# Kernel tuning notes

Measured on AMD Instinct MI355X. Metric: run time of the kernel, lower is better.

## Reference

```python
import jax, jax.numpy as jnp
import numpy as np

NUM_EXPERTS = 8
TOP_K = 2
ROUTE_SCALE = 1.0
DIM = 1024
HID = 1024
B, S = 2, 4096


def setup_inputs() -> dict:
    key = jax.random.key(0)
    ks = jax.random.split(key, 9)
    sc = 0.05
    return {
        "x": jax.random.normal(ks[0], (B, S, DIM), dtype=jnp.float32),
        "gate_w": jax.random.normal(ks[1], (NUM_EXPERTS, DIM), dtype=jnp.float32) * sc,
        "w1": jax.random.normal(ks[2], (NUM_EXPERTS, HID, DIM), dtype=jnp.float32) * sc,
        "w2": jax.random.normal(ks[3], (NUM_EXPERTS, DIM, HID), dtype=jnp.float32) * sc,
        "w3": jax.random.normal(ks[4], (NUM_EXPERTS, HID, DIM), dtype=jnp.float32) * sc,
        "sw1": jax.random.normal(ks[5], (HID, DIM), dtype=jnp.float32) * sc,
        "sw2": jax.random.normal(ks[6], (DIM, HID), dtype=jnp.float32) * sc,
        "sw3": jax.random.normal(ks[7], (HID, DIM), dtype=jnp.float32) * sc,
        "expert_bias": jnp.zeros((NUM_EXPERTS,), dtype=jnp.float32),
    }


def reference(x, gate_w, w1, w2, w3, sw1, sw2, sw3, expert_bias):
    bs, slen, dim = x.shape
    xf = x.reshape(-1, dim)                      # [T, D]

    # ---- router (sigmoid scoring, top-k over scores + bias, gather true scores) ----
    scores = jax.nn.sigmoid((xf @ gate_w.T).astype(jnp.float32))   # [T, E]
    _, sel = jax.lax.top_k(scores + expert_bias[None, :], TOP_K)    # [T, K] int32
    top_scores = jnp.take_along_axis(scores, sel, axis=1) * ROUTE_SCALE  # [T, K]

    # ---- stable sort token-slots by chosen expert (dispatch permutation) ----
    flat_sel = sel.reshape(-1)                       # [T*K]
    order = jnp.argsort(flat_sel, stable=True)       # [T*K]
    scores_sorted = top_scores.reshape(-1)[order]    # [T*K]
    tok_idx = order // TOP_K                         # source token per slot
    expert_ids = flat_sel[order]                     # sorted expert id per slot

    routed = xf[tok_idx]                             # gather [T*K, D]
    # score_before_experts=True: scale inputs by routing score
    routed = (routed.astype(jnp.float32) * scores_sorted[:, None]).astype(x.dtype)

    # ---- grouped expert GLU MLP (loop over fixed expert count, masked) ----
    out_r = jnp.zeros_like(routed)
    for e in range(NUM_EXPERTS):
        m = (expert_ids == e)[:, None]
        h = jax.nn.silu(routed @ w1[e].T) * (routed @ w3[e].T)   # [T*K, H]
        out_r = out_r + jnp.where(m, h @ w2[e].T, jnp.zeros((), routed.dtype))

    # ---- shared expert on all tokens ----
    shared = (jax.nn.silu(xf @ sw1.T) * (xf @ sw3.T)) @ sw2.T    # [T, D]

    # NOTE: original code multiplies by routing scores again after experts
    # (in addition to score_before_experts) -- replicated faithfully.
    out_r = (out_r.astype(jnp.float32) * scores_sorted[:, None]).astype(x.dtype)

    out = shared.at[tok_idx].add(out_r)              # scatter-add combine
    return out.reshape(bs, slen, dim)
```

## Files before the change

### kernel.cpp

```cpp
#include <hip/hip_runtime.h>
#include <stdint.h>

typedef unsigned short u16;
typedef unsigned int u32;

#define T_TOK 8192
#define DIMSZ 1024
#define HIDSZ 1024
#define NE 8
#define NSLOT (T_TOK * 2)

typedef __attribute__((ext_vector_type(8))) __bf16 bf16x8;
typedef __attribute__((ext_vector_type(4))) float f32x4;

__device__ __forceinline__ int sw_idx(int row, int kc) {
  return row * 32 + ((kc ^ (row & 3)) * 8);
}

__device__ __forceinline__ u16 f2bf(float f) {
  u32 u = __builtin_bit_cast(u32, f);
  u += 0x7FFFu + ((u >> 16) & 1u);
  return (u16)(u >> 16);
}
__device__ __forceinline__ float bflo(u32 v) { return __builtin_bit_cast(float, v << 16); }
__device__ __forceinline__ float bfhi(u32 v) { return __builtin_bit_cast(float, v & 0xffff0000u); }
__device__ __forceinline__ u32 pack2(float a, float b) {
  return (u32)f2bf(a) | ((u32)f2bf(b) << 16);
}
__device__ __forceinline__ float silu_f(float v) { return v / (1.f + expf(-v)); }

__global__ __launch_bounds__(256) void convert3_kernel(
    const float* __restrict__ s0, const float* __restrict__ s1,
    const float* __restrict__ s2, u16* __restrict__ d0, u16* __restrict__ d1,
    u16* __restrict__ d2, int n4) {
  const float* s = (blockIdx.y == 0) ? s0 : (blockIdx.y == 1) ? s1 : s2;
  u16* d = (blockIdx.y == 0) ? d0 : (blockIdx.y == 1) ? d1 : d2;
  int stride = gridDim.x * 256;
  for (int i = blockIdx.x * 256 + threadIdx.x; i < n4; i += stride) {
    float4 v = ((const float4*)s)[i];
    uint2 p;
    p.x = pack2(v.x, v.y);
    p.y = pack2(v.z, v.w);
    ((uint2*)d)[i] = p;
  }
}

__global__ __launch_bounds__(256) void router_kernel(
    const float* __restrict__ x, const float* __restrict__ gw,
    const float* __restrict__ bias, int* __restrict__ sel,
    float* __restrict__ selscore, u16* __restrict__ xb) {
  int t = blockIdx.x * 4 + (threadIdx.x >> 6);
  int lane = threadIdx.x & 63;
  float a[NE];
#pragma unroll
  for (int e = 0; e < NE; e++) a[e] = 0.f;
#pragma unroll
  for (int j = 0; j < 4; j++) {
    int c = j * 256 + lane * 4;
    float4 xv = *(const float4*)&x[(size_t)t * DIMSZ + c];
    uint2 p;
    p.x = pack2(xv.x, xv.y);
    p.y = pack2(xv.z, xv.w);
    *(uint2*)&xb[(size_t)t * DIMSZ + c] = p;
#pragma unroll
    for (int e = 0; e < NE; e++) {
      float4 gv = *(const float4*)&gw[e * DIMSZ + c];
      a[e] = fmaf(xv.x, gv.x, fmaf(xv.y, gv.y, fmaf(xv.z, gv.z, fmaf(xv.w, gv.w, a[e]))));
    }
  }
#pragma unroll
  for (int off = 1; off < 64; off <<= 1)
#pragma unroll
    for (int e = 0; e < NE; e++) a[e] += __shfl_xor(a[e], off);
  if (lane == 0) {
    float s[NE], b[NE];
#pragma unroll
    for (int e = 0; e < NE; e++) {
      s[e] = 1.f / (1.f + expf(-a[e]));
      b[e] = s[e] + bias[e];
    }
    int e1 = 0; float v1 = b[0];
#pragma unroll
    for (int e = 1; e < NE; e++) if (b[e] > v1) { v1 = b[e]; e1 = e; }
    int e2 = -1; float v2 = -1e30f;
#pragma unroll
    for (int e = 0; e < NE; e++) if (e != e1 && b[e] > v2) { v2 = b[e]; e2 = e; }
    sel[t * 2] = e1; sel[t * 2 + 1] = e2;
    selscore[t * 2] = s[e1];
    selscore[t * 2 + 1] = s[e2];
  }
}

__global__ __launch_bounds__(1024) void rank_kernel(
    const int* __restrict__ sel, const float* __restrict__ selscore,
    int* __restrict__ slot2pos, float* __restrict__ slot_score,
    int* __restrict__ counts, int* __restrict__ offsets) {
  __shared__ int hist[NE * 1024];
  __shared__ int tot[NE];
  __shared__ int offs[NE];
  int tid = threadIdx.x;
  int sl[16];
  int h[NE];
#pragma unroll
  for (int e = 0; e < NE; e++) h[e] = 0;
#pragma unroll
  for (int j = 0; j < 4; j++) {
    int4 v = ((const int4*)sel)[tid * 4 + j];
    sl[j * 4 + 0] = v.x; sl[j * 4 + 1] = v.y;
    sl[j * 4 + 2] = v.z; sl[j * 4 + 3] = v.w;
  }
#pragma unroll
  for (int i = 0; i < 16; i++)
#pragma unroll
    for (int e = 0; e < NE; e++) h[e] += (sl[i] == e) ? 1 : 0;
#pragma unroll
  for (int e = 0; e < NE; e++) hist[e * 1024 + tid] = h[e];
  __syncthreads();
  int wid = tid >> 6, lane = tid & 63;
  if (wid < NE) {
    int e = wid;
    int vals[16];
    int lsum = 0;
#pragma unroll
    for (int i = 0; i < 16; i++) {
      int v = hist[e * 1024 + lane * 16 + i];
      vals[i] = lsum;
      lsum += v;
    }
    int incl = lsum;
#pragma unroll
    for (int off = 1; off < 64; off <<= 1) {
      int v = __shfl_up(incl, off);
      if (lane >= off) incl += v;
    }
    int excl = incl - lsum;
#pragma unroll
    for (int i = 0; i < 16; i++) hist[e * 1024 + lane * 16 + i] = vals[i] + excl;
    if (lane == 63) tot[e] = incl;
  }
  __syncthreads();
  if (tid == 0) {
    int acc = 0;
    for (int e = 0; e < NE; e++) {
      offs[e] = acc;
      offsets[e] = acc;
      counts[e] = tot[e];
      acc += tot[e];
    }
  }
  __syncthreads();
  int base[NE];
#pragma unroll
  for (int e = 0; e < NE; e++) base[e] = offs[e] + hist[e * 1024 + tid];
#pragma unroll
  for (int i = 0; i < 16; i++) {
    int slot = tid * 16 + i;
    int e = sl[i];
    int pos = 0;
#pragma unroll
    for (int k = 0; k < NE; k++) pos += (e == k) ? base[k] : 0;
#pragma unroll
    for (int k = 0; k < NE; k++) base[k] += (e == k) ? 1 : 0;
    slot2pos[slot] = pos;
    slot_score[pos] = selscore[slot];
  }
}

__global__ __launch_bounds__(256) void gather_kernel(
    const float* __restrict__ x, const float* __restrict__ selscore,
    const int* __restrict__ slot2pos, u16* __restrict__ routed) {
  int s = blockIdx.x * 4 + (threadIdx.x >> 6);
  int lane = threadIdx.x & 63;
  int pos = slot2pos[s];
  float sc = selscore[s];
  int t = s >> 1;
#pragma unroll
  for (int j = 0; j < 4; j++) {
    int c = j * 256 + lane * 4;
    float4 v = *(const float4*)&x[(size_t)t * DIMSZ + c];
    uint2 p;
    p.x = pack2(v.x * sc, v.y * sc);
    p.y = pack2(v.z * sc, v.w * sc);
    *(uint2*)&routed[(size_t)pos * DIMSZ + c] = p;
  }
}

__global__ __launch_bounds__(256) void dual_glu_gemm(
    const u16* __restrict__ A, const u16* __restrict__ W1,
    const u16* __restrict__ W3, u16* __restrict__ Hout,
    const int* __restrict__ seg_off, const int* __restrict__ seg_cnt, int fullM) {
  int z = blockIdx.z;
  int soff = 0, scnt = fullM;
  if (seg_off) { soff = seg_off[z]; scnt = seg_cnt[z]; }
  int mbase = blockIdx.y * 128;
  if (mbase >= scnt) return;
  int nbase = blockIdx.x * 64;
  const u16* w1p = W1 + (size_t)z * HIDSZ * DIMSZ;
  const u16* w3p = W3 + (size_t)z * HIDSZ * DIMSZ;

  __shared__ u16 lA[128 * 32];
  __shared__ u16 lB1[64 * 32];
  __shared__ u16 lB3[64 * 32];

  int tid = threadIdx.x;
  int lane = tid & 63;
  int wid = tid >> 6;
  int wy = wid >> 1, wx = wid & 1;
  int q = lane >> 4, lm = lane & 15;

  f32x4 acc1[4][2], acc3[4][2];
#pragma unroll
  for (int i = 0; i < 4; i++)
#pragma unroll
    for (int j = 0; j < 2; j++) { acc1[i][j] = (f32x4)0.f; acc3[i][j] = (f32x4)0.f; }

  int arow = tid >> 2, akc = tid & 3;
  int rg0 = min(mbase + arow, scnt - 1);
  int rg1 = min(mbase + arow + 64, scnt - 1);
  const u16* gA0 = A + (size_t)(soff + rg0) * DIMSZ + akc * 8;
  const u16* gA1 = A + (size_t)(soff + rg1) * DIMSZ + akc * 8;
  const u16* gB1 = w1p + (size_t)(nbase + arow) * DIMSZ + akc * 8;
  const u16* gB3 = w3p + (size_t)(nbase + arow) * DIMSZ + akc * 8;
  int sA0 = sw_idx(arow, akc), sA1 = sw_idx(arow + 64, akc);
  int sB = sw_idx(arow, akc);

  for (int kt = 0; kt < DIMSZ / 32; kt++) {
    uint4 vA0 = *(const uint4*)gA0;
    uint4 vA1 = *(const uint4*)gA1;
    uint4 vB1 = *(const uint4*)gB1;
    uint4 vB3 = *(const uint4*)gB3;
    gA0 += 32; gA1 += 32; gB1 += 32; gB3 += 32;
    *(uint4*)&lA[sA0] = vA0;
    *(uint4*)&lA[sA1] = vA1;
    *(uint4*)&lB1[sB] = vB1;
    *(uint4*)&lB3[sB] = vB3;
    __syncthreads();
    bf16x8 af[4];
#pragma unroll
    for (int i = 0; i < 4; i++) {
      int row = wy * 64 + i * 16 + lm;
      af[i] = *(const bf16x8*)&lA[sw_idx(row, q)];
    }
    bf16x8 b1f[2], b3f[2];
#pragma unroll
    for (int j = 0; j < 2; j++) {
      int col = wx * 32 + j * 16 + lm;
      b1f[j] = *(const bf16x8*)&lB1[sw_idx(col, q)];
      b3f[j] = *(const bf16x8*)&lB3[sw_idx(col, q)];
    }
#pragma unroll
    for (int i = 0; i < 4; i++)
#pragma unroll
      for (int j = 0; j < 2; j++) {
        acc1[i][j] = __builtin_amdgcn_mfma_f32_16x16x32_bf16(af[i], b1f[j], acc1[i][j], 0, 0, 0);
        acc3[i][j] = __builtin_amdgcn_mfma_f32_16x16x32_bf16(af[i], b3f[j], acc3[i][j], 0, 0, 0);
      }
    __syncthreads();
  }
#pragma unroll
  for (int i = 0; i < 4; i++) {
    int rowb = mbase + wy * 64 + i * 16 + q * 4;
#pragma unroll
    for (int j = 0; j < 2; j++) {
      int col = nbase + wx * 32 + j * 16 + lm;
      f32x4 g1 = acc1[i][j], g3 = acc3[i][j];
#pragma unroll
      for (int r = 0; r < 4; r++) {
        int grow = rowb + r;
        if (grow < scnt)
          Hout[(size_t)(soff + grow) * HIDSZ + col] = f2bf(silu_f(g1[r]) * g3[r]);
      }
    }
  }
}

template <bool OUT_BF16>
__global__ __launch_bounds__(256) void gemm2_kernel(
    const u16* __restrict__ A, const u16* __restrict__ W, void* __restrict__ Out,
    const float* __restrict__ scale, const int* __restrict__ seg_off,
    const int* __restrict__ seg_cnt, int fullM) {
  int z = blockIdx.z;
  int soff = 0, scnt = fullM;
  if (seg_off) { soff = seg_off[z]; scnt = seg_cnt[z]; }
  int mbase = blockIdx.y * 128;
  if (mbase >= scnt) return;
  int nbase = blockIdx.x * 128;
  const u16* wp = W + (size_t)z * DIMSZ * HIDSZ;

  __shared__ u16 lA[128 * 32];
  __shared__ u16 lB[128 * 32];

  int tid = threadIdx.x;
  int lane = tid & 63;
  int wid = tid >> 6;
  int wy = wid >> 1, wx = wid & 1;
  int q = lane >> 4, lm = lane & 15;

  f32x4 acc[4][4];
#pragma unroll
  for (int i = 0; i < 4; i++)
#pragma unroll
    for (int j = 0; j < 4; j++) acc[i][j] = (f32x4)0.f;

  int arow = tid >> 2, akc = tid & 3;
  int rg0 = min(mbase + arow, scnt - 1);
  int rg1 = min(mbase + arow + 64, scnt - 1);
  const u16* gA0 = A + (size_t)(soff + rg0) * HIDSZ + akc * 8;
  const u16* gA1 = A + (size_t)(soff + rg1) * HIDSZ + akc * 8;
  const u16* gB0 = wp + (size_t)(nbase + arow) * HIDSZ + akc * 8;
  const u16* gB1 = wp + (size_t)(nbase + arow + 64) * HIDSZ + akc * 8;
  int s0 = sw_idx(arow, akc), s1 = sw_idx(arow + 64, akc);

  for (int kt = 0; kt < HIDSZ / 32; kt++) {
    uint4 vA0 = *(const uint4*)gA0;
    uint4 vA1 = *(const uint4*)gA1;
    uint4 vB0 = *(const uint4*)gB0;
    uint4 vB1 = *(const uint4*)gB1;
    gA0 += 32; gA1 += 32; gB0 += 32; gB1 += 32;
    *(uint4*)&lA[s0] = vA0;
    *(uint4*)&lA[s1] = vA1;
    *(uint4*)&lB[s0] = vB0;
    *(uint4*)&lB[s1] = vB1;
    __syncthreads();
    bf16x8 af[4], bf[4];
#pragma unroll
    for (int i = 0; i < 4; i++) {
      int row = wy * 64 + i * 16 + lm;
      int col = wx * 64 + i * 16 + lm;
      af[i] = *(const bf16x8*)&lA[sw_idx(row, q)];
      bf[i] = *(const bf16x8*)&lB[sw_idx(col, q)];
    }
#pragma unroll
    for (int i = 0; i < 4; i++)
#pragma unroll
      for (int j = 0; j < 4; j++)
        acc[i][j] = __builtin_amdgcn_mfma_f32_16x16x32_bf16(af[i], bf[j], acc[i][j], 0, 0, 0);
    __syncthreads();
  }
#pragma unroll
  for (int i = 0; i < 4; i++) {
    int rowb = mbase + wy * 64 + i * 16 + q * 4;
#pragma unroll
    for (int j = 0; j < 4; j++) {
      int col = nbase + wx * 64 + j * 16 + lm;
      f32x4 a = acc[i][j];
#pragma unroll
      for (int r = 0; r < 4; r++) {
        int grow = rowb + r;
        if (grow < scnt) {
          float s = scale ? scale[soff + grow] : 1.f;
          float v = a[r] * s;
          size_t idx = (size_t)(soff + grow) * DIMSZ + col;
          if (OUT_BF16) ((u16*)Out)[idx] = f2bf(v);
          else ((float*)Out)[idx] = v;
        }
      }
    }
  }
}

__global__ __launch_bounds__(256) void combine_kernel(
    float* __restrict__ out, const u16* __restrict__ Orb,
    const int* __restrict__ slot2pos) {
  int t = blockIdx.x;
  int d = threadIdx.x * 4;
  int p0 = slot2pos[t * 2];
  int p1 = slot2pos[t * 2 + 1];
  float4 o = *(float4*)&out[(size_t)t * DIMSZ + d];
  uint2 a = *(const uint2*)&Orb[(size_t)p0 * DIMSZ + d];
  uint2 b = *(const uint2*)&Orb[(size_t)p1 * DIMSZ + d];
  o.x += bflo(a.x) + bflo(b.x);
  o.y += bfhi(a.x) + bfhi(b.x);
  o.z += bflo(a.y) + bflo(b.y);
  o.w += bfhi(a.y) + bfhi(b.y);
  *(float4*)&out[(size_t)t * DIMSZ + d] = o;
}

extern "C" void kernel_launch(void* const* d_in, const int* in_sizes, int n_in,
                              void* d_out, int out_size, void* d_ws, size_t ws_size,
                              hipStream_t stream) {
  const float* x = (const float*)d_in[0];
  const float* gw = (const float*)d_in[1];
  const float* w1 = (const float*)d_in[2];
  const float* w2 = (const float*)d_in[3];
  const float* w3 = (const float*)d_in[4];
  const float* sw1 = (const float*)d_in[5];
  const float* sw2 = (const float*)d_in[6];
  const float* sw3 = (const float*)d_in[7];
  const float* bias = (const float*)d_in[8];
  float* out = (float*)d_out;

  uint8_t* ws = (uint8_t*)d_ws;
  size_t off = 0;
  auto alloc = [&](size_t b) { size_t o = off; off += (b + 255) & ~(size_t)255; return o; };

  size_t ctrl = alloc(256);
  int* counts = (int*)(ws + ctrl);
  int* offsets = counts + 16;
  int* sel = (int*)(ws + alloc((size_t)NSLOT * 4));
  float* selscore = (float*)(ws + alloc((size_t)NSLOT * 4));
  float* slot_score = (float*)(ws + alloc((size_t)NSLOT * 4));
  int* slot2pos = (int*)(ws + alloc((size_t)NSLOT * 4));
  u16* xb = (u16*)(ws + alloc((size_t)T_TOK * DIMSZ * 2));
  u16* routed = (u16*)(ws + alloc((size_t)NSLOT * DIMSZ * 2));
  u16* Hbuf = (u16*)(ws + alloc((size_t)NSLOT * HIDSZ * 2));
  u16* Orb = (u16*)(ws + alloc((size_t)NSLOT * DIMSZ * 2));
  u16* Hs = (u16*)(ws + alloc((size_t)T_TOK * HIDSZ * 2));
  u16* w1b = (u16*)(ws + alloc((size_t)NE * HIDSZ * DIMSZ * 2));
  u16* w2b = (u16*)(ws + alloc((size_t)NE * DIMSZ * HIDSZ * 2));
  u16* w3b = (u16*)(ws + alloc((size_t)NE * HIDSZ * DIMSZ * 2));
  u16* sw1b = (u16*)(ws + alloc((size_t)HIDSZ * DIMSZ * 2));
  u16* sw2b = (u16*)(ws + alloc((size_t)DIMSZ * HIDSZ * 2));
  u16* sw3b = (u16*)(ws + alloc((size_t)HIDSZ * DIMSZ * 2));

  convert3_kernel<<<dim3(2048, 3), 256, 0, stream>>>(
      w1, w2, w3, w1b, w2b, w3b, NE * HIDSZ * DIMSZ / 4);
  convert3_kernel<<<dim3(512, 3), 256, 0, stream>>>(
      sw1, sw2, sw3, sw1b, sw2b, sw3b, HIDSZ * DIMSZ / 4);

  router_kernel<<<T_TOK / 4, 256, 0, stream>>>(x, gw, bias, sel, selscore, xb);
  rank_kernel<<<1, 1024, 0, stream>>>(sel, selscore, slot2pos, slot_score,
                                      counts, offsets);
  gather_kernel<<<NSLOT / 4, 256, 0, stream>>>(x, selscore, slot2pos, routed);

  dual_glu_gemm<<<dim3(16, 64, 8), 256, 0, stream>>>(routed, w1b, w3b, Hbuf,
                                                     offsets, counts, 0);
  gemm2_kernel<true><<<dim3(8, 64, 8), 256, 0, stream>>>(Hbuf, w2b, (void*)Orb,
                                                         slot_score, offsets, counts, 0);
  dual_glu_gemm<<<dim3(16, 64, 1), 256, 0, stream>>>(xb, sw1b, sw3b, Hs,
                                                     nullptr, nullptr, T_TOK);
  gemm2_kernel<false><<<dim3(8, 64, 1), 256, 0, stream>>>(Hs, sw2b, (void*)d_out,
                                                          nullptr, nullptr, nullptr, T_TOK);
  combine_kernel<<<T_TOK, 256, 0, stream>>>(out, Orb, slot2pos);
}
```

Before: 523.4 us.

## Merge shared expert into grouped GEMM launches, widen GLU tile, pad LDS layout

Result: slower. 627.8 us (+20.0%).

```diff
diff --git a/kernel.cpp b/kernel.cpp
--- a/kernel.cpp
+++ b/kernel.cpp
@@ -10,12 +10,10 @@
 #define NE 8
 #define NSLOT (T_TOK * 2)
 
+#define CS 1032
+
 typedef __attribute__((ext_vector_type(8))) __bf16 bf16x8;
 typedef __attribute__((ext_vector_type(4))) float f32x4;
-
-__device__ __forceinline__ int sw_idx(int row, int kc) {
-  return row * 32 + ((kc ^ (row & 3)) * 8);
-}
 
 __device__ __forceinline__ u16 f2bf(float f) {
   u32 u = __builtin_bit_cast(u32, f);
@@ -188,19 +186,29 @@
 __global__ __launch_bounds__(256) void dual_glu_gemm(
     const u16* __restrict__ A, const u16* __restrict__ W1,
     const u16* __restrict__ W3, u16* __restrict__ Hout,
-    const int* __restrict__ seg_off, const int* __restrict__ seg_cnt, int fullM) {
+    const u16* __restrict__ As, const u16* __restrict__ SW1,
+    const u16* __restrict__ SW3, u16* __restrict__ Hs,
+    const int* __restrict__ seg_off, const int* __restrict__ seg_cnt) {
   int z = blockIdx.z;
-  int soff = 0, scnt = fullM;
-  if (seg_off) { soff = seg_off[z]; scnt = seg_cnt[z]; }
+  const u16 *Ap, *w1p, *w3p;
+  u16* Hp;
+  int soff, scnt;
+  if (z < NE) {
+    soff = seg_off[z]; scnt = seg_cnt[z];
+    Ap = A; w1p = W1 + (size_t)z * HIDSZ * DIMSZ; w3p = W3 + (size_t)z * HIDSZ * DIMSZ;
+    Hp = Hout;
+  } else {
+    soff = 0; scnt = T_TOK;
+    Ap = As; w1p = SW1; w3p = SW3;
+    Hp = Hs;
+  }
   int mbase = blockIdx.y * 128;
   if (mbase >= scnt) return;
-  int nbase = blockIdx.x * 64;
-  const u16* w1p = W1 + (size_t)z * HIDSZ * DIMSZ;
-  const u16* w3p = W3 + (size_t)z * HIDSZ * DIMSZ;
-
-  __shared__ u16 lA[128 * 32];
-  __shared__ u16 lB1[64 * 32];
-  __shared__ u16 lB3[64 * 32];
+  int nbase = blockIdx.x * 128;
+
+  __shared__ u16 lA[4 * CS];
+  __shared__ u16 lB1[4 * CS];
+  __shared__ u16 lB3[4 * CS];
 
   int tid = threadIdx.x;
   int lane = tid & 63;
@@ -208,87 +216,93 @@
   int wy = wid >> 1, wx = wid & 1;
   int q = lane >> 4, lm = lane & 15;
 
-  f32x4 acc1[4][2], acc3[4][2];
+  f32x4 acc1[4][4], acc3[4][4];
 #pragma unroll
   for (int i = 0; i < 4; i++)
 #pragma unroll
-    for (int j = 0; j < 2; j++) { acc1[i][j] = (f32x4)0.f; acc3[i][j] = (f32x4)0.f; }
-
-  int arow = tid >> 2, akc = tid & 3;
-  int rg0 = min(mbase + arow, scnt - 1);
-  int rg1 = min(mbase + arow + 64, scnt - 1);
-  const u16* gA0 = A + (size_t)(soff + rg0) * DIMSZ + akc * 8;
-  const u16* gA1 = A + (size_t)(soff + rg1) * DIMSZ + akc * 8;
-  const u16* gB1 = w1p + (size_t)(nbase + arow) * DIMSZ + akc * 8;
-  const u16* gB3 = w3p + (size_t)(nbase + arow) * DIMSZ + akc * 8;
-  int sA0 = sw_idx(arow, akc), sA1 = sw_idx(arow + 64, akc);
-  int sB = sw_idx(arow, akc);
+    for (int j = 0; j < 4; j++) { acc1[i][j] = (f32x4)0.f; acc3[i][j] = (f32x4)0.f; }
+
+  int r = tid >> 2, kc = tid & 3;
+  int rg0 = min(mbase + r, scnt - 1);
+  int rg1 = min(mbase + r + 64, scnt - 1);
+  const u16* gA0 = Ap + (size_t)(soff + rg0) * DIMSZ + kc * 8;
+  const u16* gA1 = Ap + (size_t)(soff + rg1) * DIMSZ + kc * 8;
+  const u16* gB1a = w1p + (size_t)(nbase + r) * DIMSZ + kc * 8;
+  const u16* gB1b = w1p + (size_t)(nbase + r + 64) * DIMSZ + kc * 8;
+  const u16* gB3a = w3p + (size_t)(nbase + r) * DIMSZ + kc * 8;
+  const u16* gB3b = w3p + (size_t)(nbase + r + 64) * DIMSZ + kc * 8;
+  int s0 = kc * CS + r * 8, s1 = kc * CS + (r + 64) * 8;
 
   for (int kt = 0; kt < DIMSZ / 32; kt++) {
     uint4 vA0 = *(const uint4*)gA0;
     uint4 vA1 = *(const uint4*)gA1;
-    uint4 vB1 = *(const uint4*)gB1;
-    uint4 vB3 = *(const uint4*)gB3;
-    gA0 += 32; gA1 += 32; gB1 += 32; gB3 += 32;
-    *(uint4*)&lA[sA0] = vA0;
-    *(uint4*)&lA[sA1] = vA1;
-    *(uint4*)&lB1[sB] = vB1;
-    *(uint4*)&lB3[sB] = vB3;
+    uint4 vB1a = *(const uint4*)gB1a;
+    uint4 vB1b = *(const uint4*)gB1b;
+    uint4 vB3a = *(const uint4*)gB3a;
+    uint4 vB3b = *(const uint4*)gB3b;
+    gA0 += 32; gA1 += 32; gB1a += 32; gB1b += 32; gB3a += 32; gB3b += 32;
+    *(uint4*)&lA[s0] = vA0;
+    *(uint4*)&lA[s1] = vA1;
+    *(uint4*)&lB1[s0] = vB1a;
+    *(uint4*)&lB1[s1] = vB1b;
+    *(uint4*)&lB3[s0] = vB3a;
+    *(uint4*)&lB3[s1] = vB3b;
     __syncthreads();
     bf16x8 af[4];
 #pragma unroll
-    for (int i = 0; i < 4; i++) {
-      int row = wy * 64 + i * 16 + lm;
-      af[i] = *(const bf16x8*)&lA[sw_idx(row, q)];
-    }
-    bf16x8 b1f[2], b3f[2];
-#pragma unroll
-    for (int j = 0; j < 2; j++) {
-      int col = wx * 32 + j * 16 + lm;
-      b1f[j] = *(const bf16x8*)&lB1[sw_idx(col, q)];
-      b3f[j] = *(const bf16x8*)&lB3[sw_idx(col, q)];
-    }
-#pragma unroll
     for (int i = 0; i < 4; i++)
-#pragma unroll
-      for (int j = 0; j < 2; j++) {
-        acc1[i][j] = __builtin_amdgcn_mfma_f32_16x16x32_bf16(af[i], b1f[j], acc1[i][j], 0, 0, 0);
-        acc3[i][j] = __builtin_amdgcn_mfma_f32_16x16x32_bf16(af[i], b3f[j], acc3[i][j], 0, 0, 0);
+      af[i] = *(const bf16x8*)&lA[q * CS + (wy * 64 + i * 16 + lm) * 8];
+#pragma unroll
+    for (int j = 0; j < 4; j++) {
+      int col = wx * 64 + j * 16 + lm;
+      bf16x8 b1 = *(const bf16x8*)&lB1[q * CS + col * 8];
+      bf16x8 b3 = *(const bf16x8*)&lB3[q * CS + col * 8];
+#pragma unroll
+      for (int i = 0; i < 4; i++) {
+        acc1[i][j] = __builtin_amdgcn_mfma_f32_16x16x32_bf16(af[i], b1, acc1[i][j], 0, 0, 0);
+        acc3[i][j] = __builtin_amdgcn_mfma_f32_16x16x32_bf16(af[i], b3, acc3[i][j], 0, 0, 0);
       }
+    }
     __syncthreads();
   }
 #pragma unroll
   for (int i = 0; i < 4; i++) {
     int rowb = mbase + wy * 64 + i * 16 + q * 4;
 #pragma unroll
-    for (int j = 0; j < 2; j++) {
-      int col = nbase + wx * 32 + j * 16 + lm;
+    for (int j = 0; j < 4; j++) {
+      int col = nbase + wx * 64 + j * 16 + lm;
       f32x4 g1 = acc1[i][j], g3 = acc3[i][j];
 #pragma unroll
-      for (int r = 0; r < 4; r++) {
-        int grow = rowb + r;
+      for (int rr = 0; rr < 4; rr++) {
+        int grow = rowb + rr;
         if (grow < scnt)
-          Hout[(size_t)(soff + grow) * HIDSZ + col] = f2bf(silu_f(g1[r]) * g3[r]);
+          Hp[(size_t)(soff + grow) * HIDSZ + col] = f2bf(silu_f(g1[rr]) * g3[rr]);
       }
     }
   }
 }
 
-template <bool OUT_BF16>
 __global__ __launch_bounds__(256) void gemm2_kernel(
-    const u16* __restrict__ A, const u16* __restrict__ W, void* __restrict__ Out,
+    const u16* __restrict__ A, const u16* __restrict__ W, u16* __restrict__ OutB,
+    const u16* __restrict__ As, const u16* __restrict__ SW, float* __restrict__ OutF,
     const float* __restrict__ scale, const int* __restrict__ seg_off,
-    const int* __restrict__ seg_cnt, int fullM) {
+    const int* __restrict__ seg_cnt) {
   int z = blockIdx.z;
-  int soff = 0, scnt = fullM;
-  if (seg_off) { soff = seg_off[z]; scnt = seg_cnt[z]; }
+  const u16 *Ap, *wp;
+  int soff, scnt;
+  if (z < NE) {
+    soff = seg_off[z]; scnt = seg_cnt[z];
+    Ap = A; wp = W + (size_t)z * DIMSZ * HIDSZ;
+  } else {
+    soff = 0; scnt = T_TOK;
+    Ap = As; wp = SW;
+  }
   int mbase = blockIdx.y * 128;
   if (mbase >= scnt) return;
   int nbase = blockIdx.x * 128;
-  const u16* wp = W + (size_t)z * DIMSZ * HIDSZ;
-
-  __shared__ u16 lA[128 * 32];
-  __shared__ u16 lB[128 * 32];
+
+  __shared__ u16 lA[4 * CS];
+  __shared__ u16 lB[4 * CS];
 
   int tid = threadIdx.x;
   int lane = tid & 63;
@@ -302,14 +316,14 @@
 #pragma unroll
     for (int j = 0; j < 4; j++) acc[i][j] = (f32x4)0.f;
 
-  int arow = tid >> 2, akc = tid & 3;
-  int rg0 = min(mbase + arow, scnt - 1);
-  int rg1 = min(mbase + arow + 64, scnt - 1);
-  const u16* gA0 = A + (size_t)(soff + rg0) * HIDSZ + akc * 8;
-  const u16* gA1 = A + (size_t)(soff + rg1) * HIDSZ + akc * 8;
-  const u16* gB0 = wp + (size_t)(nbase + arow) * HIDSZ + akc * 8;
-  const u16* gB1 = wp + (size_t)(nbase + arow + 64) * HIDSZ + akc * 8;
-  int s0 = sw_idx(arow, akc), s1 = sw_idx(arow + 64, akc);
+  int r = tid >> 2, kc = tid & 3;
+  int rg0 = min(mbase + r, scnt - 1);
+  int rg1 = min(mbase + r + 64, scnt - 1);
+  const u16* gA0 = Ap + (size_t)(soff + rg0) * HIDSZ + kc * 8;
+  const u16* gA1 = Ap + (size_t)(soff + rg1) * HIDSZ + kc * 8;
+  const u16* gB0 = wp + (size_t)(nbase + r) * HIDSZ + kc * 8;
+  const u16* gB1 = wp + (size_t)(nbase + r + 64) * HIDSZ + kc * 8;
+  int s0 = kc * CS + r * 8, s1 = kc * CS + (r + 64) * 8;
 
   for (int kt = 0; kt < HIDSZ / 32; kt++) {
     uint4 vA0 = *(const uint4*)gA0;
@@ -325,10 +339,8 @@
     bf16x8 af[4], bf[4];
 #pragma unroll
     for (int i = 0; i < 4; i++) {
-      int row = wy * 64 + i * 16 + lm;
-      int col = wx * 64 + i * 16 + lm;
-      af[i] = *(const bf16x8*)&lA[sw_idx(row, q)];
-      bf[i] = *(const bf16x8*)&lB[sw_idx(col, q)];
+      af[i] = *(const bf16x8*)&lA[q * CS + (wy * 64 + i * 16 + lm) * 8];
+      bf[i] = *(const bf16x8*)&lB[q * CS + (wx * 64 + i * 16 + lm) * 8];
     }
 #pragma unroll
     for (int i = 0; i < 4; i++)
@@ -345,14 +357,15 @@
       int col = nbase + wx * 64 + j * 16 + lm;
       f32x4 a = acc[i][j];
 #pragma unroll
-      for (int r = 0; r < 4; r++) {
-        int grow = rowb + r;
+      for (int rr = 0; rr < 4; rr++) {
+        int grow = rowb + rr;
         if (grow < scnt) {
-          float s = scale ? scale[soff + grow] : 1.f;
-          float v = a[r] * s;
           size_t idx = (size_t)(soff + grow) * DIMSZ + col;
-          if (OUT_BF16) ((u16*)Out)[idx] = f2bf(v);
-          else ((float*)Out)[idx] = v;
+          if (z < NE) {
+            OutB[idx] = f2bf(a[rr] * scale[soff + grow]);
+          } else {
+            OutF[idx] = a[rr];
+          }
         }
       }
     }
@@ -423,13 +436,10 @@
                                       counts, offsets);
   gather_kernel<<<NSLOT / 4, 256, 0, stream>>>(x, selscore, slot2pos, routed);
 
-  dual_glu_gemm<<<dim3(16, 64, 8), 256, 0, stream>>>(routed, w1b, w3b, Hbuf,
-                                                     offsets, counts, 0);
-  gemm2_kernel<true><<<dim3(8, 64, 8), 256, 0, stream>>>(Hbuf, w2b, (void*)Orb,
-                                                         slot_score, offsets, counts, 0);
-  dual_glu_gemm<<<dim3(16, 64, 1), 256, 0, stream>>>(xb, sw1b, sw3b, Hs,
-                                                     nullptr, nullptr, T_TOK);
-  gemm2_kernel<false><<<dim3(8, 64, 1), 256, 0, stream>>>(Hs, sw2b, (void*)d_out,
-                                                          nullptr, nullptr, nullptr, T_TOK);
+  dual_glu_gemm<<<dim3(8, 64, NE + 1), 256, 0, stream>>>(
+      routed, w1b, w3b, Hbuf, xb, sw1b, sw3b, Hs, offsets, counts);
+  gemm2_kernel<<<dim3(8, 64, NE + 1), 256, 0, stream>>>(
+      Hbuf, w2b, Orb, Hs, sw2b, out, slot_score, offsets, counts);
+
   combine_kernel<<<T_TOK, 256, 0, stream>>>(out, Orb, slot2pos);
 }
```
